# Kernel tuning notes

Hardware: AMD Instinct MI355X
Metric: run time of the kernel (lower is better)

The kernel has to match this reference:

```python
import jax, jax.numpy as jnp
import numpy as np

EPSILON = 0.1
ALPHA = 0.5
N_ITER = 10
N_USERS = 100000


def setup_inputs() -> dict:
    key = jax.random.key(0)
    k1, k2, k3, k4, k5, k6 = jax.random.split(key, 6)
    B, C, F = 2048, 1024, 128
    users = jax.random.randint(k1, (B,), 0, N_USERS)
    items = jax.random.randint(k2, (B, C), 0, C)
    D = jax.random.uniform(k3, (B, C), minval=0.1, maxval=1.0)
    capacities = jax.random.uniform(k4, (C,), minval=0.5, maxval=1.5)
    # ScaledEmbedding: normal init scaled down by embedding_dim
    item_emb = jax.random.normal(k5, (C, F), dtype=jnp.float32) / F
    user_emb = jax.random.normal(k6, (N_USERS, F), dtype=jnp.float32) / F
    return dict(users=users, items=items, D=D, capacities=capacities,
                item_emb=item_emb, user_emb=user_emb)


def reference(users, items, D, capacities, item_emb, user_emb):
    B, C = D.shape
    ie = item_emb[items]            # [B, C, F] gathered candidate embeddings
    ue = user_emb[users]            # [B, F]
    dot = jnp.einsum('bcf,bf->bc', ie, ue)          # batched dot products
    affinity = (1.0 - ALPHA) * dot - ALPHA * (D / jnp.mean(D))
    K = jnp.exp(affinity / EPSILON)                 # [B, C]

    scaling = B / N_USERS
    a = jnp.ones((B,), K.dtype)
    b = capacities * scaling                        # [C]

    def step(carry, _):
        _, v = carry
        u = a / (K @ v)                             # [B]
        v_new = b / (K.T @ u)                       # [C]
        return (u, v_new), None

    (u, v), _ = jax.lax.scan(step, (a, jnp.ones((C,), K.dtype)),
                             None, length=N_ITER)
    P = K * (u[:, None] * v[None, :])               # K * outer(u, v)
    return P
```

## Files before the change

kernel.cpp:

```cpp
#include <hip/hip_runtime.h>
#include <hip/hip_fp16.h>

#define BB      2048
#define CC      1024
#define FF      128
#define NBLK    256
#define RPB     8
#define TPB     512
#define NITER   10
#define SUBR    4
#define SCALING_F (2048.0f / 100000.0f)

#define NLEAF   8
#define LPB     32
#define NSLOT   (NITER + 1)
#define CPAD    16

__device__ unsigned g_epoch;
__device__ unsigned g_leaf[NSLOT * NLEAF * CPAD];
__device__ unsigned g_root[NSLOT * CPAD];
__device__ unsigned g_rel [NSLOT * CPAD];
__device__ float g_meanPart[NBLK];
__device__ float g_colsum[NITER * SUBR * CC];

__device__ __forceinline__ float atomLoadF(const float* p) {
    return __hip_atomic_load(p, __ATOMIC_RELAXED, __HIP_MEMORY_SCOPE_AGENT);
}
__device__ __forceinline__ void atomStoreF(float* p, float v) {
    __hip_atomic_store(p, v, __ATOMIC_RELAXED, __HIP_MEMORY_SCOPE_AGENT);
}
__device__ __forceinline__ unsigned atomAddU(unsigned* p) {
    return __hip_atomic_fetch_add(p, 1u, __ATOMIC_RELAXED,
                                  __HIP_MEMORY_SCOPE_AGENT);
}
__device__ __forceinline__ unsigned loadU(const unsigned* p) {
    return __hip_atomic_load(p, __ATOMIC_RELAXED, __HIP_MEMORY_SCOPE_AGENT);
}
__device__ __forceinline__ void storeU(unsigned* p, unsigned v) {
    __hip_atomic_store(p, v, __ATOMIC_RELAXED, __HIP_MEMORY_SCOPE_AGENT);
}

__device__ __forceinline__ void tree_barrier(int slot, unsigned e,
                                             int bid, int tid) {
    __syncthreads();
    if (tid == 0) {
        const int leaf = bid >> 5;
        unsigned rl = atomAddU(&g_leaf[(slot * NLEAF + leaf) * CPAD]);
        if (rl == e * LPB + (LPB - 1)) {
            unsigned rr = atomAddU(&g_root[slot * CPAD]);
            if (rr == e * NLEAF + (NLEAF - 1))
                storeU(&g_rel[slot * CPAD], e + 1u);
        }
        while ((int)(loadU(&g_rel[slot * CPAD]) - (e + 1u)) < 0)
            ;
    }
    __syncthreads();
}

__global__ void __launch_bounds__(TPB)
fused_sinkhorn(const int* __restrict__ users, const int* __restrict__ items,
               const float* __restrict__ D, const float* __restrict__ caps,
               const float* __restrict__ iemb, const float* __restrict__ uemb,
               float* __restrict__ out) {
    const int bid = blockIdx.x, tid = threadIdx.x;
    const int r0 = bid * RPB;

    __shared__ union { float ue[RPB][FF]; float v[CC]; } uv;
    __shared__ __half dott[RPB][CC];
    __shared__ float  Kt[RPB][CC];
    __shared__ float  ush[RPB];
    __shared__ float  red[TPB / 64];
    __shared__ float  s2sh;
    __shared__ unsigned s_epoch;

    if (tid == 0) s_epoch = atomAddU(&g_epoch) >> 8;

    const float4* Dg  = (const float4*)(D + ((size_t)r0 << 10));
    const int4*   it4 = (const int4*)(items + ((size_t)r0 << 10));
    float4 d_reg[4];
    int4   it_reg[4];
    #pragma unroll
    for (int k = 0; k < 4; ++k) d_reg[k]  = Dg[tid + k * TPB];
    #pragma unroll
    for (int k = 0; k < 4; ++k) it_reg[k] = it4[tid + k * TPB];

    const float cap0 = caps[tid]       * SCALING_F;
    const float cap1 = caps[tid + 512] * SCALING_F;

    for (int i = bid * TPB + tid; i < NITER * SUBR * CC; i += NBLK * TPB)
        atomStoreF(&g_colsum[i], 0.0f);

    if (tid < 256) {
        int r = tid >> 5, f4 = tid & 31;
        int u = users[r0 + r];
        ((float4*)uv.ue[r])[f4] = ((const float4*)(uemb + (size_t)u * FF))[f4];
    }

    float p = 0.0f;
    #pragma unroll
    for (int k = 0; k < 4; ++k) {
        float4 d = d_reg[k];
        p += d.x + d.y + d.z + d.w;
    }
    #pragma unroll
    for (int off = 32; off > 0; off >>= 1) p += __shfl_down(p, off, 64);
    if ((tid & 63) == 0) red[tid >> 6] = p;
    __syncthreads();
    const unsigned e = s_epoch;
    if (tid == 0) {
        float s = 0.0f;
        #pragma unroll
        for (int k = 0; k < TPB / 64; ++k) s += red[k];
        atomStoreF(&g_meanPart[bid], s);
    }

    if (tid < 256) {
        const float4* us  = (const float4*)uv.ue;
        const float4* ip0 = (const float4*)(iemb + (size_t)tid * FF);
        const float4* ip1 = (const float4*)(iemb + (size_t)(tid + 256) * FF);
        const float4* ip2 = (const float4*)(iemb + (size_t)(tid + 512) * FF);
        const float4* ip3 = (const float4*)(iemb + (size_t)(tid + 768) * FF);
        float acc0[RPB] = {}, acc1[RPB] = {}, acc2[RPB] = {}, acc3[RPB] = {};
        for (int f4 = 0; f4 < FF / 4; ++f4) {
            float4 a0 = ip0[f4], a1 = ip1[f4], a2 = ip2[f4], a3 = ip3[f4];
            #pragma unroll
            for (int r = 0; r < RPB; ++r) {
                float4 b = us[r * (FF / 4) + f4];
                acc0[r] += a0.x * b.x + a0.y * b.y + a0.z * b.z + a0.w * b.w;
                acc1[r] += a1.x * b.x + a1.y * b.y + a1.z * b.z + a1.w * b.w;
                acc2[r] += a2.x * b.x + a2.y * b.y + a2.z * b.z + a2.w * b.w;
                acc3[r] += a3.x * b.x + a3.y * b.y + a3.z * b.z + a3.w * b.w;
            }
        }
        #pragma unroll
        for (int r = 0; r < RPB; ++r) {
            dott[r][tid]       = __float2half(acc0[r]);
            dott[r][tid + 256] = __float2half(acc1[r]);
            dott[r][tid + 512] = __float2half(acc2[r]);
            dott[r][tid + 768] = __float2half(acc3[r]);
        }
    }

    tree_barrier(NITER, e, bid, tid);

    if (tid < 64) {
        float s = 0.0f;
        #pragma unroll
        for (int k = 0; k < NBLK / 64; ++k)
            s += atomLoadF(&g_meanPart[tid + 64 * k]);
        #pragma unroll
        for (int off = 32; off > 0; off >>= 1) s += __shfl_down(s, off, 64);
        if (tid == 0) s2sh = 5.0f * (float)(BB * CC) / s;
    }
    __syncthreads();
    const float s2 = s2sh;
    float4* KtL = (float4*)Kt;
    #pragma unroll
    for (int k = 0; k < 4; ++k) {
        int    i  = tid + k * TPB;
        int4   iv = it_reg[k];
        float4 d  = d_reg[k];
        int    r  = i >> 8;
        float4 kv;
        kv.x = __expf(5.0f * __half2float(dott[r][iv.x]) - s2 * d.x);
        kv.y = __expf(5.0f * __half2float(dott[r][iv.y]) - s2 * d.y);
        kv.z = __expf(5.0f * __half2float(dott[r][iv.z]) - s2 * d.z);
        kv.w = __expf(5.0f * __half2float(dott[r][iv.w]) - s2 * d.w);
        KtL[i] = kv;
    }

    for (int t = 0; t < NITER; ++t) {
        if (t == 0) {
            uv.v[tid]       = 1.0f;
            uv.v[tid + 512] = 1.0f;
        } else {
            const float* base = g_colsum + (size_t)(t - 1) * SUBR * CC;
            float t0[SUBR], t1[SUBR];
            #pragma unroll
            for (int k = 0; k < SUBR; ++k) t0[k] = atomLoadF(&base[k * CC + tid]);
            #pragma unroll
            for (int k = 0; k < SUBR; ++k) t1[k] = atomLoadF(&base[k * CC + tid + 512]);
            float s0 = 0.0f, s1 = 0.0f;
            #pragma unroll
            for (int k = 0; k < SUBR; ++k) { s0 += t0[k]; s1 += t1[k]; }
            uv.v[tid]       = cap0 / s0;
            uv.v[tid + 512] = cap1 / s1;
        }
        __syncthreads();

        {
            int r = tid >> 6, l = tid & 63;
            const float4* kr = (const float4*)Kt[r];
            const float4* v4 = (const float4*)uv.v;
            float pp = 0.0f;
            #pragma unroll
            for (int i2 = 0; i2 < 4; ++i2) {
                float4 k = kr[l + i2 * 64], v = v4[l + i2 * 64];
                pp += k.x * v.x + k.y * v.y + k.z * v.z + k.w * v.w;
            }
            #pragma unroll
            for (int off = 32; off > 0; off >>= 1) pp += __shfl_down(pp, off, 64);
            if (l == 0) ush[r] = 1.0f / pp;
        }
        __syncthreads();

        {
            float* cb = g_colsum + ((size_t)t * SUBR + (bid & (SUBR - 1))) * CC;
            float sA = 0.0f, sB = 0.0f;
            #pragma unroll
            for (int r = 0; r < RPB; ++r) {
                sA += Kt[r][tid]       * ush[r];
                sB += Kt[r][tid + 512] * ush[r];
            }
            atomicAdd(&cb[tid],       sA);
            atomicAdd(&cb[tid + 512], sB);
        }

        tree_barrier(t, e, bid, tid);
    }

    {
        const float* base = g_colsum + (size_t)(NITER - 1) * SUBR * CC;
        float t0[SUBR], t1[SUBR];
        #pragma unroll
        for (int k = 0; k < SUBR; ++k) t0[k] = atomLoadF(&base[k * CC + tid]);
        #pragma unroll
        for (int k = 0; k < SUBR; ++k) t1[k] = atomLoadF(&base[k * CC + tid + 512]);
        float s0 = 0.0f, s1 = 0.0f;
        #pragma unroll
        for (int k = 0; k < SUBR; ++k) { s0 += t0[k]; s1 += t1[k]; }
        uv.v[tid]       = cap0 / s0;
        uv.v[tid + 512] = cap1 / s1;
    }
    __syncthreads();

    float4* o4 = (float4*)(out + ((size_t)r0 << 10));
    #pragma unroll
    for (int k = 0; k < 4; ++k) {
        int    i  = tid + k * TPB;
        int    r  = i >> 8;
        float4 kk = KtL[i];
        float  ur = ush[r];
        float4 v  = *(const float4*)&uv.v[(i * 4) & (CC - 1)];
        float4 pv;
        pv.x = kk.x * ur * v.x;  pv.y = kk.y * ur * v.y;
        pv.z = kk.z * ur * v.z;  pv.w = kk.w * ur * v.w;
        o4[i] = pv;
    }
}

extern "C" void kernel_launch(void* const* d_in, const int* in_sizes, int n_in,
                              void* d_out, int out_size, void* d_ws, size_t ws_size,
                              hipStream_t stream) {
    const int*   users = (const int*)d_in[0];
    const int*   items = (const int*)d_in[1];
    const float* D     = (const float*)d_in[2];
    const float* caps  = (const float*)d_in[3];
    const float* iemb  = (const float*)d_in[4];
    const float* uemb  = (const float*)d_in[5];
    float* out = (float*)d_out;

    hipLaunchKernelGGL(fused_sinkhorn, dim3(NBLK), dim3(TPB), 0, stream,
                       users, items, D, caps, iemb, uemb, out);
}
```

Baseline: 191.5 us.

## Compute user-item dot products with fp16 MFMA and widen colsum sub-reduction

Replaces the scalar FMA loop that computed the 8x1024 user-item dot products with MFMA 16x16x32 fp16 instructions. User embeddings load straight into register fragments instead of going through shared memory, and item embeddings are converted to fp16 on the fly. Half of the 16 MFMA rows are zero padding because each block holds only 8 rows. SUBR also rises from 4 to 8, which spreads the column-sum atomics over more partial buffers at the cost of more loads per iteration. fp16 inputs reduce the precision of the dot products.

```diff
diff --git a/kernel.cpp b/kernel.cpp
--- a/kernel.cpp
+++ b/kernel.cpp
@@ -8,13 +8,16 @@
 #define RPB     8
 #define TPB     512
 #define NITER   10
-#define SUBR    4
+#define SUBR    8
 #define SCALING_F (2048.0f / 100000.0f)
 
 #define NLEAF   8
 #define LPB     32
 #define NSLOT   (NITER + 1)
 #define CPAD    16
+
+typedef _Float16 v8h  __attribute__((ext_vector_type(8)));
+typedef float    v4f  __attribute__((ext_vector_type(4)));
 
 __device__ unsigned g_epoch;
 __device__ unsigned g_leaf[NSLOT * NLEAF * CPAD];
@@ -64,8 +67,9 @@
                float* __restrict__ out) {
     const int bid = blockIdx.x, tid = threadIdx.x;
     const int r0 = bid * RPB;
-
-    __shared__ union { float ue[RPB][FF]; float v[CC]; } uv;
+    const int lane = tid & 63, wid = tid >> 6;
+
+    __shared__ float  vsh[CC];
     __shared__ __half dott[RPB][CC];
     __shared__ float  Kt[RPB][CC];
     __shared__ float  ush[RPB];
@@ -90,12 +94,6 @@
     for (int i = bid * TPB + tid; i < NITER * SUBR * CC; i += NBLK * TPB)
         atomStoreF(&g_colsum[i], 0.0f);
 
-    if (tid < 256) {
-        int r = tid >> 5, f4 = tid & 31;
-        int u = users[r0 + r];
-        ((float4*)uv.ue[r])[f4] = ((const float4*)(uemb + (size_t)u * FF))[f4];
-    }
-
     float p = 0.0f;
     #pragma unroll
     for (int k = 0; k < 4; ++k) {
@@ -114,30 +112,50 @@
         atomStoreF(&g_meanPart[bid], s);
     }
 
-    if (tid < 256) {
-        const float4* us  = (const float4*)uv.ue;
-        const float4* ip0 = (const float4*)(iemb + (size_t)tid * FF);
-        const float4* ip1 = (const float4*)(iemb + (size_t)(tid + 256) * FF);
-        const float4* ip2 = (const float4*)(iemb + (size_t)(tid + 512) * FF);
-        const float4* ip3 = (const float4*)(iemb + (size_t)(tid + 768) * FF);
-        float acc0[RPB] = {}, acc1[RPB] = {}, acc2[RPB] = {}, acc3[RPB] = {};
-        for (int f4 = 0; f4 < FF / 4; ++f4) {
-            float4 a0 = ip0[f4], a1 = ip1[f4], a2 = ip2[f4], a3 = ip3[f4];
-            #pragma unroll
-            for (int r = 0; r < RPB; ++r) {
-                float4 b = us[r * (FF / 4) + f4];
-                acc0[r] += a0.x * b.x + a0.y * b.y + a0.z * b.z + a0.w * b.w;
-                acc1[r] += a1.x * b.x + a1.y * b.y + a1.z * b.z + a1.w * b.w;
-                acc2[r] += a2.x * b.x + a2.y * b.y + a2.z * b.z + a2.w * b.w;
-                acc3[r] += a3.x * b.x + a3.y * b.y + a3.z * b.z + a3.w * b.w;
-            }
-        }
-        #pragma unroll
-        for (int r = 0; r < RPB; ++r) {
-            dott[r][tid]       = __float2half(acc0[r]);
-            dott[r][tid + 256] = __float2half(acc1[r]);
-            dott[r][tid + 512] = __float2half(acc2[r]);
-            dott[r][tid + 768] = __float2half(acc3[r]);
+    {
+        const int arow = lane & 15, kq = lane >> 4;
+        v8h afrag[4];
+        if (arow < RPB) {
+            int u = users[r0 + arow];
+            const float4* up = (const float4*)(uemb + (size_t)u * FF);
+            #pragma unroll
+            for (int ks = 0; ks < 4; ++ks) {
+                float4 a0 = up[ks * 8 + kq * 2];
+                float4 a1 = up[ks * 8 + kq * 2 + 1];
+                v8h a;
+                a[0] = (_Float16)a0.x; a[1] = (_Float16)a0.y;
+                a[2] = (_Float16)a0.z; a[3] = (_Float16)a0.w;
+                a[4] = (_Float16)a1.x; a[5] = (_Float16)a1.y;
+                a[6] = (_Float16)a1.z; a[7] = (_Float16)a1.w;
+                afrag[ks] = a;
+            }
+        } else {
+            #pragma unroll
+            for (int ks = 0; ks < 4; ++ks) afrag[ks] = (v8h)0;
+        }
+        #pragma unroll
+        for (int cti = 0; cti < 8; ++cti) {
+            const int ct = wid * 8 + cti;
+            const int j  = ct * 16 + arow;
+            const float4* jp = (const float4*)(iemb + (size_t)j * FF);
+            v4f acc = {0.f, 0.f, 0.f, 0.f};
+            #pragma unroll
+            for (int ks = 0; ks < 4; ++ks) {
+                float4 b0 = jp[ks * 8 + kq * 2];
+                float4 b1 = jp[ks * 8 + kq * 2 + 1];
+                v8h b;
+                b[0] = (_Float16)b0.x; b[1] = (_Float16)b0.y;
+                b[2] = (_Float16)b0.z; b[3] = (_Float16)b0.w;
+                b[4] = (_Float16)b1.x; b[5] = (_Float16)b1.y;
+                b[6] = (_Float16)b1.z; b[7] = (_Float16)b1.w;
+                acc = __builtin_amdgcn_mfma_f32_16x16x32_f16(afrag[ks], b, acc,
+                                                             0, 0, 0);
+            }
+            if (kq < 2) {
+                #pragma unroll
+                for (int i = 0; i < 4; ++i)
+                    dott[kq * 4 + i][ct * 16 + arow] = __float2half(acc[i]);
+            }
         }
     }
 
@@ -171,8 +189,8 @@
 
     for (int t = 0; t < NITER; ++t) {
         if (t == 0) {
-            uv.v[tid]       = 1.0f;
-            uv.v[tid + 512] = 1.0f;
+            vsh[tid]       = 1.0f;
+            vsh[tid + 512] = 1.0f;
         } else {
             const float* base = g_colsum + (size_t)(t - 1) * SUBR * CC;
             float t0[SUBR], t1[SUBR];
@@ -183,15 +201,15 @@
             float s0 = 0.0f, s1 = 0.0f;
             #pragma unroll
             for (int k = 0; k < SUBR; ++k) { s0 += t0[k]; s1 += t1[k]; }
-            uv.v[tid]       = cap0 / s0;
-            uv.v[tid + 512] = cap1 / s1;
+            vsh[tid]       = cap0 / s0;
+            vsh[tid + 512] = cap1 / s1;
         }
         __syncthreads();
 
         {
             int r = tid >> 6, l = tid & 63;
             const float4* kr = (const float4*)Kt[r];
-            const float4* v4 = (const float4*)uv.v;
+            const float4* v4 = (const float4*)vsh;
             float pp = 0.0f;
             #pragma unroll
             for (int i2 = 0; i2 < 4; ++i2) {
@@ -229,8 +247,8 @@
         float s0 = 0.0f, s1 = 0.0f;
         #pragma unroll
         for (int k = 0; k < SUBR; ++k) { s0 += t0[k]; s1 += t1[k]; }
-        uv.v[tid]       = cap0 / s0;
-        uv.v[tid + 512] = cap1 / s1;
+        vsh[tid]       = cap0 / s0;
+        vsh[tid + 512] = cap1 / s1;
     }
     __syncthreads();
 
@@ -241,7 +259,7 @@
         int    r  = i >> 8;
         float4 kk = KtL[i];
         float  ur = ush[r];
-        float4 v  = *(const float4*)&uv.v[(i * 4) & (CC - 1)];
+        float4 v  = *(const float4*)&vsh[(i * 4) & (CC - 1)];
         float4 pv;
         pv.x = kk.x * ur * v.x;  pv.y = kk.y * ur * v.y;
         pv.z = kk.z * ur * v.z;  pv.w = kk.w * ur * v.w;
```

New measurement: 164.0 us (median of 2 runs). -14.4%, faster.
